# Kernel tuning notes

Measured on AMD Instinct MI355X. Metric: run time of the kernel, lower is better.

The kernel has to match this reference:

```python
import jax, jax.numpy as jnp
import numpy as np

LAMBDA_SOFTMAX = 9.0
LAMBDA_LSE = 6.0
EPS = 1e-8
LEAKY_SLOPE = 0.1


def setup_inputs() -> dict:
    key = jax.random.key(0)
    k1, k2, k3, k4 = jax.random.split(key, 4)
    B, R, L, D = 256, 36, 40, 1024  # n_image=n_caption=B, n_regions, max_words, embed
    return {
        'pool_img': jax.random.normal(k1, (B, D), jnp.float32),
        'img_emb': jax.random.normal(k2, (B, R, D), jnp.float32),
        'pool_txt': jax.random.normal(k3, (B, D), jnp.float32),
        'cap_emb': jax.random.normal(k4, (B, L, D), jnp.float32),
    }


def _l2norm(x, axis):
    return x / (jnp.sqrt(jnp.sum(x * x, axis=axis, keepdims=True)) + EPS)


def _lse_reduce(m):
    # mul_(lambda_lse).exp_() ; sum over singleton dim ; log / lambda_lse
    return jnp.log(jnp.exp(m * LAMBDA_LSE)) / LAMBDA_LSE


def _text_score_one(cap_i, txt_poo_i, images):
    # cap_i: (L, d) query; images: (B, R, d) context. clipped_l2norm variant.
    attn = jnp.einsum('brd,ld->brl', images, cap_i)            # (B, R, L)
    attn = jax.nn.leaky_relu(attn, LEAKY_SLOPE)
    attn = _l2norm(attn, axis=2)                               # l2norm over queryL
    attn = jnp.swapaxes(attn, 1, 2)                            # (B, L, R)
    attn = jax.nn.softmax(attn * LAMBDA_SOFTMAX, axis=-1)      # softmax over regions
    wctx = jnp.einsum('blr,brd->bld', attn, images)            # (B, L, d)
    w12 = jnp.einsum('bld,d->bl', wctx, txt_poo_i)
    w1 = jnp.sqrt(jnp.sum(txt_poo_i * txt_poo_i))
    w2 = jnp.sqrt(jnp.sum(wctx * wctx, axis=2))
    sim = w12 / jnp.maximum(w1 * w2, EPS)                      # (B, L)
    return _lse_reduce(jnp.mean(sim, axis=1))                  # (B,)


def _image_score_one(cap_i, img_emb, img_poo):
    # query: img_emb (B, R, d); context: cap_i (L, d) broadcast over B.
    attn = jnp.einsum('ld,brd->blr', cap_i, img_emb)           # (B, L, R)
    attn = jax.nn.leaky_relu(attn, LEAKY_SLOPE)
    attn = _l2norm(attn, axis=2)                               # l2norm over regions
    attn = jnp.swapaxes(attn, 1, 2)                            # (B, R, L)
    attn = jax.nn.softmax(attn * LAMBDA_SOFTMAX, axis=-1)      # softmax over words
    wctx = jnp.einsum('brl,ld->brd', attn, cap_i)              # (B, R, d)
    w12 = jnp.einsum('brd,bd->br', wctx, img_poo)
    w1 = jnp.sqrt(jnp.sum(img_poo * img_poo, axis=1, keepdims=True))  # (B,1)
    w2 = jnp.sqrt(jnp.sum(wctx * wctx, axis=2))                # (B, R)
    sim = w12 / jnp.maximum(w1 * w2, EPS)
    return _lse_reduce(jnp.mean(sim, axis=1))                  # (B,)


def reference(pool_img, img_emb, pool_txt, cap_emb):
    # scores_t2i: loop over captions -> vmap; result (n_cap, n_image) -> transpose
    t2i = jax.vmap(_text_score_one, in_axes=(0, 0, None))(cap_emb, pool_txt, img_emb).T
    i2t = jax.vmap(_image_score_one, in_axes=(0, None, None))(cap_emb, img_emb, pool_img).T
    base = pool_img @ pool_txt.T
    return t2i + i2t + base
```

## Files before the change

### kernel.cpp

```cpp
#include <hip/hip_runtime.h>

typedef unsigned short u16;
typedef __attribute__((ext_vector_type(8))) short bf16x8;
typedef __attribute__((ext_vector_type(4))) float f32x4;
typedef __attribute__((ext_vector_type(2))) __fp16 h16x2;

#define D_EMB 1024
#define NBAT  256
#define AS1 __attribute__((address_space(1)))
#define AS3 __attribute__((address_space(3)))

__device__ __forceinline__ u16 f2bf(float f){
    unsigned int u = __float_as_uint(f);
    unsigned int r = (u + 0x7fffu + ((u >> 16) & 1u)) >> 16;
    return (u16)r;
}
__device__ __forceinline__ float leaky(float x){ return x > 0.f ? x : 0.1f * x; }

__device__ __forceinline__ float dot2h(h16x2 a, h16x2 b, float c){
#if __has_builtin(__builtin_amdgcn_fdot2)
    return __builtin_amdgcn_fdot2(a, b, c, false);
#else
    return fmaf((float)a[0], (float)b[0], fmaf((float)a[1], (float)b[1], c));
#endif
}

__global__ void pack_kernel(const float* __restrict__ pool_img, const float* __restrict__ img_emb,
                            const float* __restrict__ pool_txt, const float* __restrict__ cap_emb,
                            u16* __restrict__ imgw, u16* __restrict__ capw,
                            float* __restrict__ w1i, float* __restrict__ w1t){
    __shared__ float red[256];
    int row = blockIdx.x;
    const float* src; u16* dst;
    bool is_pool; float* wout;
    if (row < NBAT * 37){
        int e = row / 37, rr = row - e * 37;
        is_pool = (rr == 36);
        src = (rr < 36) ? (img_emb + ((size_t)e * 36 + rr) * D_EMB) : (pool_img + (size_t)e * D_EMB);
        dst = imgw + (size_t)row * D_EMB;
        wout = w1i + e;
    } else {
        int r2 = row - NBAT * 37;
        int e = r2 / 41, rr = r2 - e * 41;
        is_pool = (rr == 40);
        src = (rr < 40) ? (cap_emb + ((size_t)e * 40 + rr) * D_EMB) : (pool_txt + (size_t)e * D_EMB);
        dst = capw + (size_t)r2 * D_EMB;
        wout = w1t + e;
    }
    int t = threadIdx.x;
    float4 v = ((const float4*)src)[t];
    unsigned long long pk = (unsigned long long)f2bf(v.x)
        | ((unsigned long long)f2bf(v.y) << 16)
        | ((unsigned long long)f2bf(v.z) << 32)
        | ((unsigned long long)f2bf(v.w) << 48);
    *(unsigned long long*)(dst + (size_t)t * 4) = pk;
    if (is_pool){
        red[t] = v.x*v.x + v.y*v.y + v.z*v.z + v.w*v.w;
        __syncthreads();
        for (int off = 128; off > 0; off >>= 1){
            if (t < off) red[t] += red[t + off];
            __syncthreads();
        }
        if (t == 0) *wout = sqrtf(red[0]);
    }
}

__launch_bounds__(256, 2)
__global__ void gram_kernel(const u16* __restrict__ imgw, const u16* __restrict__ capw,
                            float* __restrict__ G, float* __restrict__ H){
    __shared__ __align__(16) char gsm[6144];
    int blk = blockIdx.x;
    int tid = threadIdx.x, lane = tid & 63;
    int wave = __builtin_amdgcn_readfirstlane(tid >> 6);
    int frow = lane & 15, q = lane >> 4;

    const u16* E; float* Gout; int R;
    if (blk < NBAT){ E = imgw + (size_t)blk * 37 * D_EMB; Gout = G + (size_t)blk * 1296; R = 36; }
    else { int b = blk - NBAT; E = capw + (size_t)b * 41 * D_EMB; Gout = H + (size_t)b * 1600; R = 40; }

    {
        uint4 z = {0u,0u,0u,0u};
        for (int off = tid * 16; off < 6144; off += 4096) *(uint4*)(gsm + off) = z;
    }

    const u16* gsrc[2]; int goff[2]; bool gval[2];
    #pragma unroll
    for (int j = 0; j < 2; ++j){
        int g = wave + j * 4;
        gval[j] = false; gsrc[j] = E; goff[j] = 0;
        if (g < 6){
            int kk = g / 3, t = g - kk * 3;
            int row = t * 16 + frow;
            gsrc[j] = E + (size_t)row * D_EMB + kk * 32 + q * 8;
            goff[j] = g * 1024;
            gval[j] = (row < R);
        }
    }

    int wm = wave >> 1, wn = wave & 1;
    int nTm = wm ? 1 : 2, nTn = wn ? 1 : 2;
    f32x4 acc[2][2];
    #pragma unroll
    for (int a = 0; a < 2; ++a)
        #pragma unroll
        for (int b = 0; b < 2; ++b) acc[a][b] = (f32x4){0.f,0.f,0.f,0.f};

    for (int c = 0; c < 16; ++c){
        __syncthreads();
        #pragma unroll
        for (int j = 0; j < 2; ++j){
            if (gval[j]){
                __builtin_amdgcn_global_load_lds(
                    (const AS1 void*)(const void*)(gsrc[j] + c * 64),
                    (AS3 void*)(void*)(gsm + goff[j] + lane * 16),
                    16, 0, 0);
            }
        }
        __syncthreads();
        #pragma unroll
        for (int kk = 0; kk < 2; ++kk){
            bf16x8 fA[2], fB[2];
            #pragma unroll
            for (int mi = 0; mi < 2; ++mi)
                if (mi < nTm) fA[mi] = *(const bf16x8*)(gsm + ((kk * 3 + (wm + mi * 2)) * 64 + lane) * 16);
            #pragma unroll
            for (int ni = 0; ni < 2; ++ni)
                if (ni < nTn) fB[ni] = *(const bf16x8*)(gsm + ((kk * 3 + (wn + ni * 2)) * 64 + lane) * 16);
            #pragma unroll
            for (int mi = 0; mi < 2; ++mi)
                if (mi < nTm)
                    #pragma unroll
                    for (int ni = 0; ni < 2; ++ni)
                        if (ni < nTn)
                            acc[mi][ni] = __builtin_amdgcn_mfma_f32_16x16x32_bf16(
                                fA[mi], fB[ni], acc[mi][ni], 0, 0, 0);
        }
    }

    #pragma unroll
    for (int mi = 0; mi < 2; ++mi){
        if (mi < nTm){
            int tm = wm + mi * 2;
            #pragma unroll
            for (int ni = 0; ni < 2; ++ni){
                if (ni < nTn){
                    int tn = wn + ni * 2;
                    int col = tn * 16 + frow;
                    if (col < R){
                        #pragma unroll
                        for (int g = 0; g < 4; ++g){
                            int row = tm * 16 + q * 4 + g;
                            if (row < R) Gout[row * R + col] = acc[mi][ni][g];
                        }
                    }
                }
            }
        }
    }
}

__global__ void ghpack_kernel(const float* __restrict__ G, const float* __restrict__ H,
                              h16x2* __restrict__ Gh, h16x2* __restrict__ Hh){
    int id = blockIdx.x;
    int t = threadIdx.x;
    if (id < NBAT){
        const float* src = G + (size_t)id * 1296;
        h16x2* dst = Gh + (size_t)id * 648;
        for (int i = t; i < 648; i += 256)
            dst[i] = __builtin_amdgcn_cvt_pkrtz(src[2 * i], src[2 * i + 1]);
    } else {
        const float* src = H + (size_t)(id - NBAT) * 1600;
        h16x2* dst = Hh + (size_t)(id - NBAT) * 800;
        for (int i = t; i < 800; i += 256)
            dst[i] = __builtin_amdgcn_cvt_pkrtz(src[2 * i], src[2 * i + 1]);
    }
}

__launch_bounds__(256, 5)
__global__ void fused_kernel(const u16* __restrict__ imgw, const u16* __restrict__ capw,
                             const h16x2* __restrict__ Gh, const h16x2* __restrict__ Hh,
                             const float* __restrict__ w1i, const float* __restrict__ w1t,
                             float* __restrict__ out){
    __shared__ __align__(16) char smem[26624];
    float* Call = (float*)smem;
    float* rnb  = (float*)(smem + 25160);
    float* cnb  = (float*)(smem + 25736);

    int tid  = threadIdx.x;
    int lane = tid & 63;
    int wave = __builtin_amdgcn_readfirstlane(tid >> 6);
    int frow = lane & 15, q = lane >> 4;

    int lin = blockIdx.x;
    int xcd = lin & 7;
    int s   = lin >> 3;
    int b_t = (xcd << 4) | (s & 15);
    int i_t = s >> 4;
    int b0 = b_t * 2, i0 = i_t * 2;
    const u16* Ag = imgw + (size_t)b0 * 37 * D_EMB;
    const u16* Bg = capw + (size_t)i0 * 41 * D_EMB;

    {
        uint4 z = {0u,0u,0u,0u};
        for (int off = tid * 16; off < 22528; off += 4096) *(uint4*)(smem + off) = z;
    }

    const u16* gsrc[6]; int goff[6]; bool gval[6];
    #pragma unroll
    for (int j = 0; j < 6; ++j){
        int g = wave + j * 4;
        gval[j] = false; gsrc[j] = Ag; goff[j] = 0;
        if (g < 22){
            if (g < 10){
                int tm = g % 5, kk = g / 5;
                int row = tm * 16 + frow;
                gsrc[j] = Ag + (size_t)row * D_EMB + kk * 32 + q * 8;
                goff[j] = g * 1024;
                gval[j] = (row < 74);
            } else {
                int gb = g - 10;
                int tn = gb % 6, kk = gb / 6;
                int row = tn * 16 + frow;
                gsrc[j] = Bg + (size_t)row * D_EMB + kk * 32 + q * 8;
                goff[j] = 10240 + gb * 1024;
                gval[j] = (row < 82);
            }
        }
    }

    int wm = wave >> 1, wn = wave & 1;
    int nTm = wm ? 2 : 3;
    f32x4 acc[3][3];
    #pragma unroll
    for (int aa = 0; aa < 3; ++aa)
        #pragma unroll
        for (int bb = 0; bb < 3; ++bb) acc[aa][bb] = (f32x4){0.f, 0.f, 0.f, 0.f};

    for (int c = 0; c < 16; ++c){
        __syncthreads();
        #pragma unroll
        for (int j = 0; j < 6; ++j){
            if (gval[j]){
                __builtin_amdgcn_global_load_lds(
                    (const AS1 void*)(const void*)(gsrc[j] + c * 64),
                    (AS3 void*)(void*)(smem + goff[j] + lane * 16),
                    16, 0, 0);
            }
        }
        __syncthreads();
        #pragma unroll
        for (int kk = 0; kk < 2; ++kk){
            bf16x8 bfr[3];
            #pragma unroll
            for (int ni = 0; ni < 3; ++ni){
                int tn = wn + ni * 2;
                bfr[ni] = *(const bf16x8*)(smem + 10240 + ((kk * 6 + tn) * 64 + lane) * 16);
            }
            #pragma unroll
            for (int mi = 0; mi < 3; ++mi){
                if (mi < nTm){
                    int tm = wm + mi * 2;
                    bf16x8 af = *(const bf16x8*)(smem + ((kk * 5 + tm) * 64 + lane) * 16);
                    #pragma unroll
                    for (int ni = 0; ni < 3; ++ni){
                        acc[mi][ni] = __builtin_amdgcn_mfma_f32_16x16x32_bf16(
                            af, bfr[ni], acc[mi][ni], 0, 0, 0);
                    }
                }
            }
        }
    }
    __syncthreads();

    #pragma unroll
    for (int mi = 0; mi < 3; ++mi){
        if (mi < nTm){
            int tm = wm + mi * 2;
            #pragma unroll
            for (int ni = 0; ni < 3; ++ni){
                int tn = wn + ni * 2;
                int col = tn * 16 + frow;
                int rbase = tm * 16 + q * 4;
                if (col < 82){
                    #pragma unroll
                    for (int g = 0; g < 4; ++g){
                        int rowc = rbase + g;
                        if (rowc < 74) Call[rowc * 85 + col] = acc[mi][ni][g];
                    }
                }
            }
        }
    }
    __syncthreads();

    int pb = wave >> 1, pi = wave & 1;
    int bg = b0 + pb, ig = i0 + pi;
    const float* Sv = Call + (pb * 37) * 85 + pi * 41;
    const h16x2* Gp = Gh + (size_t)bg * 648;
    const h16x2* Hp = Hh + (size_t)ig * 800;

    {
        int r0 = (lane < 36) ? lane : 35;
        float s2 = 0.f;
        #pragma unroll
        for (int l = 0; l < 40; ++l){ float x = leaky(Sv[r0 * 85 + l]); s2 = fmaf(x, x, s2); }
        if (lane < 36) rnb[wave * 36 + lane] = 9.f / (sqrtf(s2) + 1e-8f);
    }
    float t2i_sum;
    {
        int lc = (lane < 40) ? lane : 39;
        h16x2 uh[18];
        float num = 0.f;
        #pragma unroll
        for (int r = 0; r < 36; r += 2){
            float e0 = __expf(leaky(Sv[r * 85 + lc] * rnb[wave * 36 + r]));
            float e1 = __expf(leaky(Sv[(r + 1) * 85 + lc] * rnb[wave * 36 + r + 1]));
            num = fmaf(e0, Sv[r * 85 + 40], fmaf(e1, Sv[(r + 1) * 85 + 40], num));
            uh[r >> 1] = __builtin_amdgcn_cvt_pkrtz(e0, e1);
        }
        float zz = 0.f;
        #pragma unroll
        for (int rr = 0; rr < 36; ++rr){
            float w = 0.f;
            #pragma unroll
            for (int j = 0; j < 18; ++j)
                w = dot2h(uh[j], Gp[rr * 18 + j], w);
            zz = fmaf((float)uh[rr >> 1][rr & 1], w, zz);
        }
        float w2s = sqrtf(fmaxf(zz, 0.f));
        float sim = num / fmaxf(w1t[ig] * w2s, 1e-8f);
        sim = (lane < 40) ? sim : 0.f;
        #pragma unroll
        for (int off = 32; off > 0; off >>= 1) sim += __shfl_down(sim, off);
        t2i_sum = sim;
    }

    {
        int l0 = (lane < 40) ? lane : 39;
        float s2 = 0.f;
        #pragma unroll
        for (int r = 0; r < 36; ++r){ float x = leaky(Sv[r * 85 + l0]); s2 = fmaf(x, x, s2); }
        if (lane < 40) cnb[wave * 40 + lane] = 9.f / (sqrtf(s2) + 1e-8f);
    }
    float i2t_sum;
    {
        int rc = (lane < 36) ? lane : 35;
        h16x2 vh[20];
        float num = 0.f;
        #pragma unroll
        for (int l = 0; l < 40; l += 2){
            float e0 = __expf(leaky(Sv[rc * 85 + l] * cnb[wave * 40 + l]));
            float e1 = __expf(leaky(Sv[rc * 85 + l + 1] * cnb[wave * 40 + l + 1]));
            num = fmaf(e0, Sv[36 * 85 + l], fmaf(e1, Sv[36 * 85 + l + 1], num));
            vh[l >> 1] = __builtin_amdgcn_cvt_pkrtz(e0, e1);
        }
        float zz = 0.f;
        #pragma unroll
        for (int ll = 0; ll < 40; ++ll){
            float w = 0.f;
            #pragma unroll
            for (int j = 0; j < 20; ++j)
                w = dot2h(vh[j], Hp[ll * 20 + j], w);
            zz = fmaf((float)vh[ll >> 1][ll & 1], w, zz);
        }
        float w2s = sqrtf(fmaxf(zz, 0.f));
        float sim = num / fmaxf(w1i[bg] * w2s, 1e-8f);
        sim = (lane < 36) ? sim : 0.f;
        #pragma unroll
        for (int off = 32; off > 0; off >>= 1) sim += __shfl_down(sim, off);
        i2t_sum = sim;
    }

    if (lane == 0)
        out[bg * 256 + ig] = t2i_sum * (1.f / 40.f) + i2t_sum * (1.f / 36.f) + Sv[36 * 85 + 40];
}

extern "C" void kernel_launch(void* const* d_in, const int* in_sizes, int n_in,
                              void* d_out, int out_size, void* d_ws, size_t ws_size,
                              hipStream_t stream){
    const float* pool_img = (const float*)d_in[0];
    const float* img_emb  = (const float*)d_in[1];
    const float* pool_txt = (const float*)d_in[2];
    const float* cap_emb  = (const float*)d_in[3];
    float* out = (float*)d_out;

    char* ws = (char*)d_ws;
    size_t o = 0;
    u16* imgw = (u16*)(ws + o);  o += (size_t)256 * 37 * 1024 * 2;
    u16* capw = (u16*)(ws + o);  o += (size_t)256 * 41 * 1024 * 2;
    float* G  = (float*)(ws + o); o += (size_t)256 * 36 * 36 * 4;
    float* H  = (float*)(ws + o); o += (size_t)256 * 40 * 40 * 4;
    float* w1i = (float*)(ws + o); o += 1024;
    float* w1t = (float*)(ws + o); o += 1024;
    h16x2* Gh = (h16x2*)(ws + o); o += (size_t)256 * 648 * 4;
    h16x2* Hh = (h16x2*)(ws + o); o += (size_t)256 * 800 * 4;

    pack_kernel<<<19968, 256, 0, stream>>>(pool_img, img_emb, pool_txt, cap_emb,
                                           imgw, capw, w1i, w1t);
    gram_kernel<<<512, 256, 0, stream>>>(imgw, capw, G, H);
    ghpack_kernel<<<512, 256, 0, stream>>>(G, H, Gh, Hh);
    fused_kernel<<<16384, 256, 0, stream>>>(imgw, capw, Gh, Hh, w1i, w1t, out);
}
```

Baseline: 722.1 us.

## Exploit Gram symmetry in quadratic form and fuse fp16 packing into gram kernel

The gram kernel now writes fp16-packed Gram matrices directly, which removes the separate ghpack kernel launch and the fp32 intermediate round trip. The quadratic forms u^T G u in the fused kernel now use only the upper triangle of the symmetric Gram matrix. Diagonal terms are handled explicitly and off-diagonal sums are doubled, roughly halving the dot2 work, and two accumulators add ILP. Occupancy hint raised from 5 to 6 blocks, which risks register pressure and spills.

```diff
diff --git a/kernel.cpp b/kernel.cpp
--- a/kernel.cpp
+++ b/kernel.cpp
@@ -67,16 +67,16 @@
 
 __launch_bounds__(256, 2)
 __global__ void gram_kernel(const u16* __restrict__ imgw, const u16* __restrict__ capw,
-                            float* __restrict__ G, float* __restrict__ H){
+                            h16x2* __restrict__ Gh, h16x2* __restrict__ Hh){
     __shared__ __align__(16) char gsm[6144];
     int blk = blockIdx.x;
     int tid = threadIdx.x, lane = tid & 63;
     int wave = __builtin_amdgcn_readfirstlane(tid >> 6);
     int frow = lane & 15, q = lane >> 4;
 
-    const u16* E; float* Gout; int R;
-    if (blk < NBAT){ E = imgw + (size_t)blk * 37 * D_EMB; Gout = G + (size_t)blk * 1296; R = 36; }
-    else { int b = blk - NBAT; E = capw + (size_t)b * 41 * D_EMB; Gout = H + (size_t)b * 1600; R = 40; }
+    const u16* E; h16x2* Ghout; int R, NP;
+    if (blk < NBAT){ E = imgw + (size_t)blk * 37 * D_EMB; Ghout = Gh + (size_t)blk * 648; R = 36; NP = 18; }
+    else { int b = blk - NBAT; E = capw + (size_t)b * 41 * D_EMB; Ghout = Hh + (size_t)b * 800; R = 40; NP = 20; }
 
     {
         uint4 z = {0u,0u,0u,0u};
@@ -146,11 +146,14 @@
                 if (ni < nTn){
                     int tn = wn + ni * 2;
                     int col = tn * 16 + frow;
+                    int rbase = tm * 16 + q * 4;
                     if (col < R){
                         #pragma unroll
-                        for (int g = 0; g < 4; ++g){
-                            int row = tm * 16 + q * 4 + g;
-                            if (row < R) Gout[row * R + col] = acc[mi][ni][g];
+                        for (int gg = 0; gg < 4; gg += 2){
+                            int r0 = rbase + gg;
+                            if (r0 + 1 < R)
+                                Ghout[col * NP + (r0 >> 1)] =
+                                    __builtin_amdgcn_cvt_pkrtz(acc[mi][ni][gg], acc[mi][ni][gg + 1]);
                         }
                     }
                 }
@@ -159,24 +162,7 @@
     }
 }
 
-__global__ void ghpack_kernel(const float* __restrict__ G, const float* __restrict__ H,
-                              h16x2* __restrict__ Gh, h16x2* __restrict__ Hh){
-    int id = blockIdx.x;
-    int t = threadIdx.x;
-    if (id < NBAT){
-        const float* src = G + (size_t)id * 1296;
-        h16x2* dst = Gh + (size_t)id * 648;
-        for (int i = t; i < 648; i += 256)
-            dst[i] = __builtin_amdgcn_cvt_pkrtz(src[2 * i], src[2 * i + 1]);
-    } else {
-        const float* src = H + (size_t)(id - NBAT) * 1600;
-        h16x2* dst = Hh + (size_t)(id - NBAT) * 800;
-        for (int i = t; i < 800; i += 256)
-            dst[i] = __builtin_amdgcn_cvt_pkrtz(src[2 * i], src[2 * i + 1]);
-    }
-}
-
-__launch_bounds__(256, 5)
+__launch_bounds__(256, 6)
 __global__ void fused_kernel(const u16* __restrict__ imgw, const u16* __restrict__ capw,
                              const h16x2* __restrict__ Gh, const h16x2* __restrict__ Hh,
                              const float* __restrict__ w1i, const float* __restrict__ w1t,
@@ -321,11 +307,22 @@
         float zz = 0.f;
         #pragma unroll
         for (int rr = 0; rr < 36; ++rr){
-            float w = 0.f;
-            #pragma unroll
-            for (int j = 0; j < 18; ++j)
-                w = dot2h(uh[j], Gp[rr * 18 + j], w);
-            zz = fmaf((float)uh[rr >> 1][rr & 1], w, zz);
+            int t = rr >> 1;
+            float w0 = 0.f, w1 = 0.f;
+            #pragma unroll
+            for (int j = t + 1; j < 18; ++j){
+                if ((j - t) & 1) w0 = dot2h(uh[j], Gp[rr * 18 + j], w0);
+                else             w1 = dot2h(uh[j], Gp[rr * 18 + j], w1);
+            }
+            h16x2 dp = Gp[rr * 18 + t];
+            float tail = w0 + w1;
+            if ((rr & 1) == 0){
+                float u0 = (float)uh[t][0], u1v = (float)uh[t][1];
+                zz = fmaf(u0, fmaf((float)dp[0], u0, 2.f * fmaf((float)dp[1], u1v, tail)), zz);
+            } else {
+                float u1v = (float)uh[t][1];
+                zz = fmaf(u1v, fmaf((float)dp[1], u1v, 2.f * tail), zz);
+            }
         }
         float w2s = sqrtf(fmaxf(zz, 0.f));
         float sim = num / fmaxf(w1t[ig] * w2s, 1e-8f);
@@ -357,11 +354,22 @@
         float zz = 0.f;
         #pragma unroll
         for (int ll = 0; ll < 40; ++ll){
-            float w = 0.f;
-            #pragma unroll
-            for (int j = 0; j < 20; ++j)
-                w = dot2h(vh[j], Hp[ll * 20 + j], w);
-            zz = fmaf((float)vh[ll >> 1][ll & 1], w, zz);
+            int t = ll >> 1;
+            float w0 = 0.f, w1 = 0.f;
+            #pragma unroll
+            for (int j = t + 1; j < 20; ++j){
+                if ((j - t) & 1) w0 = dot2h(vh[j], Hp[ll * 20 + j], w0);
+                else             w1 = dot2h(vh[j], Hp[ll * 20 + j], w1);
+            }
+            h16x2 dp = Hp[ll * 20 + t];
+            float tail = w0 + w1;
+            if ((ll & 1) == 0){
+                float v0 = (float)vh[t][0], v1 = (float)vh[t][1];
+                zz = fmaf(v0, fmaf((float)dp[0], v0, 2.f * fmaf((float)dp[1], v1, tail)), zz);
+            } else {
+                float v1 = (float)vh[t][1];
+                zz = fmaf(v1, fmaf((float)dp[1], v1, 2.f * tail), zz);
+            }
         }
         float w2s = sqrtf(fmaxf(zz, 0.f));
         float sim = num / fmaxf(w1i[bg] * w2s, 1e-8f);
@@ -388,8 +396,6 @@
     size_t o = 0;
     u16* imgw = (u16*)(ws + o);  o += (size_t)256 * 37 * 1024 * 2;
     u16* capw = (u16*)(ws + o);  o += (size_t)256 * 41 * 1024 * 2;
-    float* G  = (float*)(ws + o); o += (size_t)256 * 36 * 36 * 4;
-    float* H  = (float*)(ws + o); o += (size_t)256 * 40 * 40 * 4;
     float* w1i = (float*)(ws + o); o += 1024;
     float* w1t = (float*)(ws + o); o += 1024;
     h16x2* Gh = (h16x2*)(ws + o); o += (size_t)256 * 648 * 4;
@@ -397,7 +403,6 @@
 
     pack_kernel<<<19968, 256, 0, stream>>>(pool_img, img_emb, pool_txt, cap_emb,
                                            imgw, capw, w1i, w1t);
-    gram_kernel<<<512, 256, 0, stream>>>(imgw, capw, G, H);
-    ghpack_kernel<<<512, 256, 0, stream>>>(G, H, Gh, Hh);
+    gram_kernel<<<512, 256, 0, stream>>>(imgw, capw, Gh, Hh);
     fused_kernel<<<16384, 256, 0, stream>>>(imgw, capw, Gh, Hh, w1i, w1t, out);
 }
```

Result: slower. 892.1 us (+23.5%).
